# Kernel tuning notes

Hardware: AMD Instinct MI355X
Metric: run time of the kernel (lower is better)

## Reference

```python
import jax, jax.numpy as jnp
import numpy as np

ALPHA = 32.0 ** 2
EPS = 1e-5
SCALE = 64 ** (-0.5)  # dim_head ** -0.5
HEADS = 8


def stable_softmax(t, alpha=ALPHA):
    t = t / alpha
    t = t - jax.lax.stop_gradient(jnp.max(t, axis=-1, keepdims=True))
    return jax.nn.softmax(t * alpha, axis=-1)


def setup_inputs() -> dict:
    key = jax.random.key(0)
    k1, k2, k3 = jax.random.split(key, 3)
    dim, inner = 512, 8 * 64
    x = jax.random.normal(k1, (8, dim, 32, 32), dtype=jnp.float32)
    gamma = jnp.ones((1, dim, 1, 1), dtype=jnp.float32)
    # conv2d 1x1 weights, stored as [out_ch, in_ch]
    w_qkv = jax.random.normal(k2, (inner * 3, dim), dtype=jnp.float32) * (dim ** -0.5)
    w_out = jax.random.normal(k3, (dim, inner), dtype=jnp.float32) * (inner ** -0.5)
    return {"x": x, "gamma": gamma, "w_qkv": w_qkv, "w_out": w_out}


def reference(x, gamma, w_qkv, w_out):
    b, c, H, W = x.shape
    residual = x
    # LayerNormChan: normalize over channel dim (biased variance), scale by gamma
    mean = jnp.mean(x, axis=1, keepdims=True)
    var = jnp.var(x, axis=1, keepdims=True)
    xn = (x - mean) / jnp.sqrt(var + EPS) * gamma
    # 1x1 conv QKV projection
    qkv = jnp.einsum('oc,bchw->bohw', w_qkv, xn)
    q, k, v = jnp.split(qkv, 3, axis=1)
    n = H * W
    def to_heads(t):
        return t.reshape(b, HEADS, -1, n)  # b h c (x y)
    q, k, v = map(to_heads, (q, k, v))
    sim = jnp.einsum('bhci,bhcj->bhij', q, k) * SCALE
    attn = stable_softmax(sim)
    out = jnp.einsum('bhij,bhcj->bhci', attn, v)
    out = out.reshape(b, -1, H, W)  # b (h c) x y
    out = jnp.einsum('oc,bchw->bohw', w_out, out)
    return out + residual
```

## Files before the change

### kernel.cpp

```cpp
#include <hip/hip_runtime.h>
#include <hip/hip_bf16.h>

#define NDIM   512
#define NPOS   1024
#define NB     8
#define INNER  1536
#define DHEAD  64

typedef __attribute__((ext_vector_type(8))) short bf8v;
typedef __attribute__((ext_vector_type(4))) float f4v;

__device__ __forceinline__ f4v mfma16(bf8v a, bf8v b, f4v c) {
    return __builtin_amdgcn_mfma_f32_16x16x32_bf16(a, b, c, 0, 0, 0);
}

__device__ __forceinline__ unsigned short f2bs(float v) {
    __hip_bfloat16 h = __float2bfloat16(v);
    return *reinterpret_cast<unsigned short*>(&h);
}

__device__ __forceinline__ void gl_lds16(const unsigned short* g, unsigned short* l) {
    __builtin_amdgcn_global_load_lds(
        (const __attribute__((address_space(1))) void*)g,
        (__attribute__((address_space(3))) void*)l,
        16, 0, 0);
}

__global__ __launch_bounds__(256) void prep_kernel(
    const float* __restrict__ x, const float* __restrict__ gamma,
    const float* __restrict__ wq, const float* __restrict__ wo,
    unsigned short* __restrict__ xnT, unsigned short* __restrict__ wqb,
    unsigned short* __restrict__ wob)
{
    const int blk = blockIdx.x;
    const int t = threadIdx.x;
    if (blk >= 128) {
        const int n1 = INNER * NDIM / 4;
        int i = (blk - 128) * 256 + t;
        const float* src; unsigned short* dst; int j;
        if (i < n1) { src = wq; dst = wqb; j = i; }
        else        { src = wo; dst = wob; j = i - n1; }
        float4 v = ((const float4*)src)[j];
        ushort4 u;
        u.x = f2bs(v.x); u.y = f2bs(v.y); u.z = f2bs(v.z); u.w = f2bs(v.w);
        ((ushort4*)dst)[j] = u;
        return;
    }
    __shared__ float ssum[4][64];
    __shared__ float ssq[4][64];
    __shared__ float mean_s[64];
    __shared__ float rstd_s[64];
    __shared__ unsigned short tile[64][72];

    const int b = blk >> 4;
    const int n0 = (blk & 15) * 64;
    {
        const int ln = t & 63, cg = t >> 6;
        const float* xp = x + (size_t)b * NDIM * NPOS + n0 + ln;
        float s = 0.f, ss = 0.f;
        for (int c = cg * 128; c < cg * 128 + 128; ++c) {
            float v = xp[(size_t)c * NPOS];
            s += v; ss += v * v;
        }
        ssum[cg][ln] = s; ssq[cg][ln] = ss;
    }
    __syncthreads();
    if (t < 64) {
        float st = ssum[0][t] + ssum[1][t] + ssum[2][t] + ssum[3][t];
        float sq = ssq[0][t] + ssq[1][t] + ssq[2][t] + ssq[3][t];
        float m = st * (1.0f / NDIM);
        float var = sq * (1.0f / NDIM) - m * m;
        mean_s[t] = m;
        rstd_s[t] = rsqrtf(var + 1e-5f);
    }
    __syncthreads();

    const int cl = t >> 2, nq = (t & 3) * 16;
    const int n = t >> 2, cq = (t & 3) * 16;
    for (int c0 = 0; c0 < NDIM; c0 += 64) {
        const float g = gamma[c0 + cl];
        const float* xp = x + ((size_t)b * NDIM + c0 + cl) * NPOS + n0 + nq;
#pragma unroll
        for (int q = 0; q < 4; ++q) {
            float4 v = *(const float4*)(xp + q * 4);
            float4 m = *(const float4*)&mean_s[nq + q * 4];
            float4 r = *(const float4*)&rstd_s[nq + q * 4];
            tile[nq + q * 4 + 0][cl] = f2bs((v.x - m.x) * r.x * g);
            tile[nq + q * 4 + 1][cl] = f2bs((v.y - m.y) * r.y * g);
            tile[nq + q * 4 + 2][cl] = f2bs((v.z - m.z) * r.z * g);
            tile[nq + q * 4 + 3][cl] = f2bs((v.w - m.w) * r.w * g);
        }
        __syncthreads();
        unsigned short* dst = xnT + ((size_t)b * NPOS + n0 + n) * NDIM + c0 + cq;
        *(uint4*)dst       = *(const uint4*)&tile[n][cq];
        *(uint4*)(dst + 8) = *(const uint4*)&tile[n][cq + 8];
        __syncthreads();
    }
}

__global__ __launch_bounds__(256) void qkv_mfma_kernel(
    const unsigned short* __restrict__ wq, const unsigned short* __restrict__ xnT,
    unsigned short* __restrict__ qT, unsigned short* __restrict__ kT,
    unsigned short* __restrict__ vv)
{
    __shared__ __align__(16) unsigned short smem[4 * 64 * 72];

    const int b = blockIdx.z;
    const int m0 = blockIdx.y * 128, n0 = blockIdx.x * 128;
    const int t = threadIdx.x, w = t >> 6, lane = t & 63;
    const int l15 = lane & 15, quad = lane >> 4;
    const int wm = (w >> 1) * 64, wn = (w & 1) * 64;
    const unsigned short* Abase = wq + (size_t)m0 * NDIM;
    const unsigned short* Bbase = xnT + ((size_t)b * NPOS + n0) * NDIM;

    const int rl = lane >> 2, sl = lane & 3;
    const int cw = (sl ^ ((rl >> 1) & 3)) * 8;
    const int sA = (quad ^ ((l15 >> 1) & 3)) * 8;

    f4v acc[4][4];
#pragma unroll
    for (int i = 0; i < 4; ++i)
#pragma unroll
        for (int j = 0; j < 4; ++j) { acc[i][j][0]=0.f; acc[i][j][1]=0.f; acc[i][j][2]=0.f; acc[i][j][3]=0.f; }

#pragma unroll
    for (int e = 0; e < 2; ++e) {
        const int seg = w * 2 + e;
        const int r = seg * 16 + rl;
        gl_lds16(Abase + (size_t)r * NDIM + cw, smem + seg * 512);
        gl_lds16(Bbase + (size_t)r * NDIM + cw, smem + 4096 + seg * 512);
    }

    for (int k0 = 0; k0 < NDIM; k0 += 32) {
        const int cur = (k0 >> 5) & 1;
        unsigned short* At = smem + cur * 8192;
        unsigned short* Bt = At + 4096;
        __syncthreads();
        if (k0 + 32 < NDIM) {
            unsigned short* An = smem + (cur ^ 1) * 8192;
#pragma unroll
            for (int e = 0; e < 2; ++e) {
                const int seg = w * 2 + e;
                const int r = seg * 16 + rl;
                gl_lds16(Abase + (size_t)r * NDIM + k0 + 32 + cw, An + seg * 512);
                gl_lds16(Bbase + (size_t)r * NDIM + k0 + 32 + cw, An + 4096 + seg * 512);
            }
        }
        bf8v af[4], bfr[4];
#pragma unroll
        for (int ms = 0; ms < 4; ++ms) af[ms]  = *(const bf8v*)&At[(wm + ms * 16 + l15) * 32 + sA];
#pragma unroll
        for (int ns = 0; ns < 4; ++ns) bfr[ns] = *(const bf8v*)&Bt[(wn + ns * 16 + l15) * 32 + sA];
#pragma unroll
        for (int ms = 0; ms < 4; ++ms)
#pragma unroll
            for (int ns = 0; ns < 4; ++ns)
                acc[ms][ns] = mfma16(af[ms], bfr[ns], acc[ms][ns]);
    }
    __syncthreads();

    const int sec = m0 >> 9;
    const int om  = m0 & 511;
    if (sec == 2) {
        unsigned short* vbase = vv + ((size_t)b * NDIM + om) * NPOS + n0;
#pragma unroll
        for (int ms = 0; ms < 4; ++ms)
#pragma unroll
            for (int r = 0; r < 4; ++r) {
                int m = wm + ms * 16 + quad * 4 + r;
#pragma unroll
                for (int ns = 0; ns < 4; ++ns)
                    vbase[(size_t)m * NPOS + wn + ns * 16 + l15] = f2bs(acc[ms][ns][r]);
            }
    } else {
        const float qsc = (sec == 0) ? 0.125f : 1.0f;
        unsigned short* gT = (sec == 0 ? qT : kT) + ((size_t)b * NPOS + n0) * NDIM + om;
        unsigned short (*bw)[72] = (unsigned short(*)[72])(smem + w * 64 * 72);
#pragma unroll
        for (int ms = 0; ms < 4; ++ms)
#pragma unroll
            for (int ns = 0; ns < 4; ++ns)
#pragma unroll
                for (int r = 0; r < 4; ++r)
                    bw[ns * 16 + l15][ms * 16 + quad * 4 + r] = f2bs(acc[ms][ns][r] * qsc);
        unsigned short* dst = gT + (size_t)(wn + lane) * NDIM + wm;
#pragma unroll
        for (int q2 = 0; q2 < 8; ++q2)
            *(uint4*)(dst + q2 * 8) = *(const uint4*)&bw[lane][q2 * 8];
    }
}

__global__ __launch_bounds__(256, 2) void attn_mfma8_kernel(
    const unsigned short* __restrict__ qT, const unsigned short* __restrict__ kT,
    const unsigned short* __restrict__ vv, unsigned short* __restrict__ attnT)
{
    __shared__ __align__(16) unsigned short Kb[2][4096];
    __shared__ __align__(16) unsigned short Vb[2][4096];
    __shared__ __align__(16) unsigned short Ps[4][32][72];

    const int blk = blockIdx.x;
    const int xg = blk & 7, rr = blk >> 3;
    const int i0 = (rr & 7) * 128;
    const int bh = ((rr >> 3) << 3) | xg;
    const int b = bh >> 3, h = bh & 7;

    const int t = threadIdx.x, w = t >> 6, lane = t & 63;
    const int l15 = lane & 15, quad = lane >> 4;

    const unsigned short* kbase = kT + (size_t)b * NPOS * NDIM + h * DHEAD;
    const unsigned short* vbase = vv + ((size_t)b * NDIM + h * DHEAD) * NPOS;

    bf8v bq[2][2];
#pragma unroll
    for (int g = 0; g < 2; ++g) {
        const unsigned short* qrow =
            qT + ((size_t)b * NPOS + i0 + w * 32 + g * 16 + l15) * NDIM + h * DHEAD;
        bq[g][0] = *(const bf8v*)(qrow + quad * 8);
        bq[g][1] = *(const bf8v*)(qrow + 32 + quad * 8);
    }

    bf8v bones;
#pragma unroll
    for (int e = 0; e < 8; ++e) bones[e] = (short)0x3F80;

    const int rloc = lane >> 3;
    const int gch = ((lane & 7) ^ (rloc & 7)) * 8;
    const int sw0 = (quad ^ (l15 & 7)) * 8;
    const int sw1 = ((4 + quad) ^ (l15 & 7)) * 8;

#pragma unroll
    for (int e = 0; e < 2; ++e) {
        const int seg = w * 2 + e;
        const int row = seg * 8 + rloc;
        gl_lds16(kbase + (size_t)row * NDIM + gch, &Kb[0][seg * 512]);
        gl_lds16(vbase + (size_t)row * NPOS + gch, &Vb[0][seg * 512]);
    }

    f4v oc[2][5];
#pragma unroll
    for (int mg = 0; mg < 2; ++mg)
#pragma unroll
        for (int cs = 0; cs < 5; ++cs) { oc[mg][cs][0]=0.f; oc[mg][cs][1]=0.f; oc[mg][cs][2]=0.f; oc[mg][cs][3]=0.f; }

#pragma unroll 2
    for (int j0 = 0; j0 < NPOS; j0 += 64) {
        const int cur = (j0 >> 6) & 1, nxt = cur ^ 1;
        __syncthreads();
        if (j0 + 64 < NPOS) {
#pragma unroll
            for (int e = 0; e < 2; ++e) {
                const int seg = w * 2 + e;
                const int row = seg * 8 + rloc;
                gl_lds16(kbase + (size_t)(j0 + 64 + row) * NDIM + gch, &Kb[nxt][seg * 512]);
                gl_lds16(vbase + (size_t)row * NPOS + j0 + 64 + gch, &Vb[nxt][seg * 512]);
            }
        }

#pragma unroll
        for (int jt = 0; jt < 4; ++jt) {
            const int krow = (jt * 16 + l15) * 64;
            bf8v ak0 = *(const bf8v*)&Kb[cur][krow + sw0];
            bf8v ak1 = *(const bf8v*)&Kb[cur][krow + sw1];
#pragma unroll
            for (int g = 0; g < 2; ++g) {
                f4v s; s[0]=0.f; s[1]=0.f; s[2]=0.f; s[3]=0.f;
                s = mfma16(ak0, bq[g][0], s);
                s = mfma16(ak1, bq[g][1], s);
                ushort4 pu;
                pu.x = f2bs(__expf(fminf(s[0], 60.f)));
                pu.y = f2bs(__expf(fminf(s[1], 60.f)));
                pu.z = f2bs(__expf(fminf(s[2], 60.f)));
                pu.w = f2bs(__expf(fminf(s[3], 60.f)));
                *(ushort4*)&Ps[w][g * 16 + l15][jt * 16 + quad * 4] = pu;
            }
        }
        bf8v ap[2][2];
#pragma unroll
        for (int mg = 0; mg < 2; ++mg) {
            ap[mg][0] = *(const bf8v*)&Ps[w][mg * 16 + l15][quad * 8];
            ap[mg][1] = *(const bf8v*)&Ps[w][mg * 16 + l15][32 + quad * 8];
        }
#pragma unroll
        for (int cs = 0; cs < 4; ++cs) {
            const int vrow = (cs * 16 + l15) * 64;
            bf8v bv0 = *(const bf8v*)&Vb[cur][vrow + sw0];
            bf8v bv1 = *(const bf8v*)&Vb[cur][vrow + sw1];
#pragma unroll
            for (int mg = 0; mg < 2; ++mg) {
                oc[mg][cs] = mfma16(ap[mg][0], bv0, oc[mg][cs]);
                oc[mg][cs] = mfma16(ap[mg][1], bv1, oc[mg][cs]);
            }
        }
#pragma unroll
        for (int mg = 0; mg < 2; ++mg) {
            oc[mg][4] = mfma16(ap[mg][0], bones, oc[mg][4]);
            oc[mg][4] = mfma16(ap[mg][1], bones, oc[mg][4]);
        }
    }

#pragma unroll
    for (int mg = 0; mg < 2; ++mg) {
        float inv[4];
#pragma unroll
        for (int r = 0; r < 4; ++r) inv[r] = 1.0f / oc[mg][4][r];
        unsigned short* dst =
            attnT + ((size_t)b * NPOS + i0 + w * 32 + mg * 16) * NDIM + h * DHEAD;
#pragma unroll
        for (int cs = 0; cs < 4; ++cs)
#pragma unroll
            for (int r = 0; r < 4; ++r)
                dst[(size_t)(quad * 4 + r) * NDIM + cs * 16 + l15] = f2bs(oc[mg][cs][r] * inv[r]);
    }
}

__global__ __launch_bounds__(256) void out_mfma_kernel(
    const unsigned short* __restrict__ wo, const unsigned short* __restrict__ attnT,
    const float* __restrict__ x, float* __restrict__ outp)
{
    __shared__ __align__(16) unsigned short smem[12288];

    const int b = blockIdx.z;
    const int m0 = blockIdx.y * 64, n0 = blockIdx.x * 128;
    const int t = threadIdx.x, w = t >> 6, lane = t & 63;
    const int l15 = lane & 15, quad = lane >> 4;
    const int wm = (w >> 1) * 32, wn = (w & 1) * 64;
    const unsigned short* Abase = wo + (size_t)m0 * NDIM;
    const unsigned short* Bbase = attnT + ((size_t)b * NPOS + n0) * NDIM;

    const int rl = lane >> 2, sl = lane & 3;
    const int cw = (sl ^ ((rl >> 1) & 3)) * 8;
    const int sA = (quad ^ ((l15 >> 1) & 3)) * 8;

    f4v acc[2][4];
#pragma unroll
    for (int i = 0; i < 2; ++i)
#pragma unroll
        for (int j = 0; j < 4; ++j) { acc[i][j][0]=0.f; acc[i][j][1]=0.f; acc[i][j][2]=0.f; acc[i][j][3]=0.f; }

    {
        const int r = w * 16 + rl;
        gl_lds16(Abase + (size_t)r * NDIM + cw, smem + w * 512);
#pragma unroll
        for (int e = 0; e < 2; ++e) {
            const int seg = w * 2 + e;
            const int rb = seg * 16 + rl;
            gl_lds16(Bbase + (size_t)rb * NDIM + cw, smem + 2048 + seg * 512);
        }
    }

    for (int k0 = 0; k0 < NDIM; k0 += 32) {
        const int cur = (k0 >> 5) & 1;
        unsigned short* At = smem + cur * 6144;
        unsigned short* Bt = At + 2048;
        __syncthreads();
        if (k0 + 32 < NDIM) {
            unsigned short* An = smem + (cur ^ 1) * 6144;
            const int r = w * 16 + rl;
            gl_lds16(Abase + (size_t)r * NDIM + k0 + 32 + cw, An + w * 512);
#pragma unroll
            for (int e = 0; e < 2; ++e) {
                const int seg = w * 2 + e;
                const int rb = seg * 16 + rl;
                gl_lds16(Bbase + (size_t)rb * NDIM + k0 + 32 + cw, An + 2048 + seg * 512);
            }
        }
        bf8v af[2], bfr[4];
#pragma unroll
        for (int ms = 0; ms < 2; ++ms) af[ms]  = *(const bf8v*)&At[(wm + ms * 16 + l15) * 32 + sA];
#pragma unroll
        for (int ns = 0; ns < 4; ++ns) bfr[ns] = *(const bf8v*)&Bt[(wn + ns * 16 + l15) * 32 + sA];
#pragma unroll
        for (int ms = 0; ms < 2; ++ms)
#pragma unroll
            for (int ns = 0; ns < 4; ++ns)
                acc[ms][ns] = mfma16(af[ms], bfr[ns], acc[ms][ns]);
    }
    const float* xb = x + ((size_t)b * NDIM + m0) * NPOS + n0;
    float* ob = outp + ((size_t)b * NDIM + m0) * NPOS + n0;
#pragma unroll
    for (int ms = 0; ms < 2; ++ms)
#pragma unroll
        for (int r = 0; r < 4; ++r) {
            int m = wm + ms * 16 + quad * 4 + r;
#pragma unroll
            for (int ns = 0; ns < 4; ++ns) {
                int n = wn + ns * 16 + l15;
                ob[(size_t)m * NPOS + n] = acc[ms][ns][r] + xb[(size_t)m * NPOS + n];
            }
        }
}

extern "C" void kernel_launch(void* const* d_in, const int* in_sizes, int n_in,
                              void* d_out, int out_size, void* d_ws, size_t ws_size,
                              hipStream_t stream) {
    const float* x     = (const float*)d_in[0];
    const float* gamma = (const float*)d_in[1];
    const float* w_qkv = (const float*)d_in[2];
    const float* w_out = (const float*)d_in[3];
    float* out = (float*)d_out;

    unsigned short* xnT = (unsigned short*)d_ws;
    unsigned short* wqb = xnT + (size_t)NB * NPOS * NDIM;
    unsigned short* wob = wqb + (size_t)INNER * NDIM;
    unsigned short* qTw = wob + (size_t)NDIM * NDIM;
    unsigned short* kTw = qTw + (size_t)NB * NPOS * NDIM;
    unsigned short* vvw = kTw + (size_t)NB * NPOS * NDIM;
    unsigned short* aTw = vvw + (size_t)NB * NPOS * NDIM;

    prep_kernel<<<128 + (INNER * NDIM + NDIM * NDIM) / 4 / 256, 256, 0, stream>>>(
        x, gamma, w_qkv, w_out, xnT, wqb, wob);
    qkv_mfma_kernel<<<dim3(NPOS / 128, INNER / 128, NB), 256, 0, stream>>>(
        wqb, xnT, qTw, kTw, vvw);
    attn_mfma8_kernel<<<512, 256, 0, stream>>>(qTw, kTw, vvw, aTw);
    out_mfma_kernel<<<dim3(NPOS / 128, NDIM / 64, NB), 256, 0, stream>>>(wob, aTw, x, out);
}
```

Before: 147.1 us.

## Retile layernorm prep, stage V stores through LDS, use exp2 and setprio in attention

The layernorm prep kernel now gives each block 32 positions instead of 64, doubling the block count, and writes one 16-byte store per thread. The QKV epilogue stages the V output through LDS so rows are written with coalesced 16-byte stores, and Q/K stores are remapped for better coalescing. The attention softmax folds log2(e) into the Q scale and calls the hardware exp2 directly. MFMA sections are wrapped in s_setprio to favour matrix issue across waves. The exp2 change shifts the clamp threshold and bf16 rounding slightly.

```diff
diff --git a/kernel.cpp b/kernel.cpp
--- a/kernel.cpp
+++ b/kernel.cpp
@@ -34,9 +34,9 @@
 {
     const int blk = blockIdx.x;
     const int t = threadIdx.x;
-    if (blk >= 128) {
+    if (blk >= 256) {
         const int n1 = INNER * NDIM / 4;
-        int i = (blk - 128) * 256 + t;
+        int i = (blk - 256) * 256 + t;
         const float* src; unsigned short* dst; int j;
         if (i < n1) { src = wq; dst = wqb; j = i; }
         else        { src = wo; dst = wob; j = i - n1; }
@@ -46,28 +46,30 @@
         ((ushort4*)dst)[j] = u;
         return;
     }
-    __shared__ float ssum[4][64];
-    __shared__ float ssq[4][64];
-    __shared__ float mean_s[64];
-    __shared__ float rstd_s[64];
-    __shared__ unsigned short tile[64][72];
-
-    const int b = blk >> 4;
-    const int n0 = (blk & 15) * 64;
+    __shared__ float ssum[8][32];
+    __shared__ float ssq[8][32];
+    __shared__ float mean_s[32];
+    __shared__ float rstd_s[32];
+    __shared__ unsigned short tile[32][72];
+
+    const int b = blk >> 5;
+    const int n0 = (blk & 31) * 32;
     {
-        const int ln = t & 63, cg = t >> 6;
+        const int ln = t & 31, cg = t >> 5;
         const float* xp = x + (size_t)b * NDIM * NPOS + n0 + ln;
         float s = 0.f, ss = 0.f;
-        for (int c = cg * 128; c < cg * 128 + 128; ++c) {
+#pragma unroll 8
+        for (int c = cg * 64; c < cg * 64 + 64; ++c) {
             float v = xp[(size_t)c * NPOS];
             s += v; ss += v * v;
         }
         ssum[cg][ln] = s; ssq[cg][ln] = ss;
     }
     __syncthreads();
-    if (t < 64) {
-        float st = ssum[0][t] + ssum[1][t] + ssum[2][t] + ssum[3][t];
-        float sq = ssq[0][t] + ssq[1][t] + ssq[2][t] + ssq[3][t];
+    if (t < 32) {
+        float st = 0.f, sq = 0.f;
+#pragma unroll
+        for (int g = 0; g < 8; ++g) { st += ssum[g][t]; sq += ssq[g][t]; }
         float m = st * (1.0f / NDIM);
         float var = sq * (1.0f / NDIM) - m * m;
         mean_s[t] = m;
@@ -75,25 +77,28 @@
     }
     __syncthreads();
 
-    const int cl = t >> 2, nq = (t & 3) * 16;
-    const int n = t >> 2, cq = (t & 3) * 16;
+    const int cl = t >> 2, nq = (t & 3) * 8;
+    const int nr = t >> 3, ch = (t & 7) * 8;
     for (int c0 = 0; c0 < NDIM; c0 += 64) {
         const float g = gamma[c0 + cl];
         const float* xp = x + ((size_t)b * NDIM + c0 + cl) * NPOS + n0 + nq;
-#pragma unroll
-        for (int q = 0; q < 4; ++q) {
-            float4 v = *(const float4*)(xp + q * 4);
-            float4 m = *(const float4*)&mean_s[nq + q * 4];
-            float4 r = *(const float4*)&rstd_s[nq + q * 4];
-            tile[nq + q * 4 + 0][cl] = f2bs((v.x - m.x) * r.x * g);
-            tile[nq + q * 4 + 1][cl] = f2bs((v.y - m.y) * r.y * g);
-            tile[nq + q * 4 + 2][cl] = f2bs((v.z - m.z) * r.z * g);
-            tile[nq + q * 4 + 3][cl] = f2bs((v.w - m.w) * r.w * g);
-        }
+        float4 v0 = *(const float4*)(xp);
+        float4 v1 = *(const float4*)(xp + 4);
+        float4 m0 = *(const float4*)&mean_s[nq];
+        float4 m1 = *(const float4*)&mean_s[nq + 4];
+        float4 r0 = *(const float4*)&rstd_s[nq];
+        float4 r1 = *(const float4*)&rstd_s[nq + 4];
+        tile[nq + 0][cl] = f2bs((v0.x - m0.x) * r0.x * g);
+        tile[nq + 1][cl] = f2bs((v0.y - m0.y) * r0.y * g);
+        tile[nq + 2][cl] = f2bs((v0.z - m0.z) * r0.z * g);
+        tile[nq + 3][cl] = f2bs((v0.w - m0.w) * r0.w * g);
+        tile[nq + 4][cl] = f2bs((v1.x - m1.x) * r1.x * g);
+        tile[nq + 5][cl] = f2bs((v1.y - m1.y) * r1.y * g);
+        tile[nq + 6][cl] = f2bs((v1.z - m1.z) * r1.z * g);
+        tile[nq + 7][cl] = f2bs((v1.w - m1.w) * r1.w * g);
         __syncthreads();
-        unsigned short* dst = xnT + ((size_t)b * NPOS + n0 + n) * NDIM + c0 + cq;
-        *(uint4*)dst       = *(const uint4*)&tile[n][cq];
-        *(uint4*)(dst + 8) = *(const uint4*)&tile[n][cq + 8];
+        unsigned short* dst = xnT + ((size_t)b * NPOS + n0 + nr) * NDIM + c0 + ch;
+        *(uint4*)dst = *(const uint4*)&tile[nr][ch];
         __syncthreads();
     }
 }
@@ -162,18 +167,24 @@
     const int sec = m0 >> 9;
     const int om  = m0 & 511;
     if (sec == 2) {
+        unsigned short (*bw)[72] = (unsigned short(*)[72])(smem + w * 64 * 72);
         unsigned short* vbase = vv + ((size_t)b * NDIM + om) * NPOS + n0;
 #pragma unroll
         for (int ms = 0; ms < 4; ++ms)
 #pragma unroll
-            for (int r = 0; r < 4; ++r) {
-                int m = wm + ms * 16 + quad * 4 + r;
-#pragma unroll
-                for (int ns = 0; ns < 4; ++ns)
-                    vbase[(size_t)m * NPOS + wn + ns * 16 + l15] = f2bs(acc[ms][ns][r]);
-            }
+            for (int ns = 0; ns < 4; ++ns)
+#pragma unroll
+                for (int r = 0; r < 4; ++r)
+                    bw[ms * 16 + quad * 4 + r][ns * 16 + l15] = f2bs(acc[ms][ns][r]);
+#pragma unroll
+        for (int r2 = 0; r2 < 4; ++r2) {
+            const int ml = r2 * 16 + (lane >> 2);
+            unsigned short* dstr = vbase + (size_t)(wm + ml) * NPOS + wn + (lane & 3) * 8;
+            *(uint4*)dstr        = *(const uint4*)&bw[ml][(lane & 3) * 8];
+            *(uint4*)(dstr + 32) = *(const uint4*)&bw[ml][32 + (lane & 3) * 8];
+        }
     } else {
-        const float qsc = (sec == 0) ? 0.125f : 1.0f;
+        const float qsc = (sec == 0) ? 0.18033688f : 1.0f;
         unsigned short* gT = (sec == 0 ? qT : kT) + ((size_t)b * NPOS + n0) * NDIM + om;
         unsigned short (*bw)[72] = (unsigned short(*)[72])(smem + w * 64 * 72);
 #pragma unroll
@@ -183,10 +194,13 @@
 #pragma unroll
                 for (int r = 0; r < 4; ++r)
                     bw[ns * 16 + l15][ms * 16 + quad * 4 + r] = f2bs(acc[ms][ns][r] * qsc);
-        unsigned short* dst = gT + (size_t)(wn + lane) * NDIM + wm;
-#pragma unroll
-        for (int q2 = 0; q2 < 8; ++q2)
-            *(uint4*)(dst + q2 * 8) = *(const uint4*)&bw[lane][q2 * 8];
+#pragma unroll
+        for (int r2 = 0; r2 < 4; ++r2) {
+            const int nl = r2 * 16 + (lane >> 2);
+            unsigned short* dstr = gT + (size_t)(wn + nl) * NDIM + wm + (lane & 3) * 8;
+            *(uint4*)dstr        = *(const uint4*)&bw[nl][(lane & 3) * 8];
+            *(uint4*)(dstr + 32) = *(const uint4*)&bw[nl][32 + (lane & 3) * 8];
+        }
     }
 }
 
@@ -264,13 +278,15 @@
 #pragma unroll
             for (int g = 0; g < 2; ++g) {
                 f4v s; s[0]=0.f; s[1]=0.f; s[2]=0.f; s[3]=0.f;
+                __builtin_amdgcn_s_setprio(1);
                 s = mfma16(ak0, bq[g][0], s);
                 s = mfma16(ak1, bq[g][1], s);
+                __builtin_amdgcn_s_setprio(0);
                 ushort4 pu;
-                pu.x = f2bs(__expf(fminf(s[0], 60.f)));
-                pu.y = f2bs(__expf(fminf(s[1], 60.f)));
-                pu.z = f2bs(__expf(fminf(s[2], 60.f)));
-                pu.w = f2bs(__expf(fminf(s[3], 60.f)));
+                pu.x = f2bs(__builtin_amdgcn_exp2f(fminf(s[0], 86.f)));
+                pu.y = f2bs(__builtin_amdgcn_exp2f(fminf(s[1], 86.f)));
+                pu.z = f2bs(__builtin_amdgcn_exp2f(fminf(s[2], 86.f)));
+                pu.w = f2bs(__builtin_amdgcn_exp2f(fminf(s[3], 86.f)));
                 *(ushort4*)&Ps[w][g * 16 + l15][jt * 16 + quad * 4] = pu;
             }
         }
@@ -280,6 +296,7 @@
             ap[mg][0] = *(const bf8v*)&Ps[w][mg * 16 + l15][quad * 8];
             ap[mg][1] = *(const bf8v*)&Ps[w][mg * 16 + l15][32 + quad * 8];
         }
+        __builtin_amdgcn_s_setprio(1);
 #pragma unroll
         for (int cs = 0; cs < 4; ++cs) {
             const int vrow = (cs * 16 + l15) * 64;
@@ -296,6 +313,7 @@
             oc[mg][4] = mfma16(ap[mg][0], bones, oc[mg][4]);
             oc[mg][4] = mfma16(ap[mg][1], bones, oc[mg][4]);
         }
+        __builtin_amdgcn_s_setprio(0);
     }
 
 #pragma unroll
@@ -407,7 +425,7 @@
     unsigned short* vvw = kTw + (size_t)NB * NPOS * NDIM;
     unsigned short* aTw = vvw + (size_t)NB * NPOS * NDIM;
 
-    prep_kernel<<<128 + (INNER * NDIM + NDIM * NDIM) / 4 / 256, 256, 0, stream>>>(
+    prep_kernel<<<256 + (INNER * NDIM + NDIM * NDIM) / 4 / 256, 256, 0, stream>>>(
         x, gamma, w_qkv, w_out, xnT, wqb, wob);
     qkv_mfma_kernel<<<dim3(NPOS / 128, INNER / 128, NB), 256, 0, stream>>>(
         wqb, xnT, qTw, kTw, vvw);
```

After: 137.5 us. 6.5% less time.
